# Kernel optimization log

Measured on AMD Instinct MI355X. Metric: run time of the kernel, lower is better.

## Reference

```python
import jax, jax.numpy as jnp
import numpy as np

D_MODEL = 1024
N_HEAD = 16
HEAD_SIZE = D_MODEL // N_HEAD
LAYER_ID = 12
N_LAYER = 24
HEAD_SIZE_DIVISOR = 8
TM_DIM = 32   # TIME_MIX_EXTRA_DIM
TD_DIM = 64   # TIME_DECAY_EXTRA_DIM
B, T = 4, 1024
EPS = 1e-5 * HEAD_SIZE_DIVISOR ** 2


def setup_inputs() -> dict:
    key = jax.random.key(0)
    ks = jax.random.split(key, 12)
    C = D_MODEL
    r0 = LAYER_ID / (N_LAYER - 1)
    r1 = 1.0 - LAYER_ID / N_LAYER
    ddd = np.arange(C, dtype=np.float64) / C
    time_maa_x = (1.0 - ddd ** r1).astype(np.float32)
    time_maa_w = (1.0 - ddd ** r1).astype(np.float32)
    time_maa_k = (1.0 - ddd ** r1).astype(np.float32)
    time_maa_v = (1.0 - (ddd ** r1 + 0.3 * r0)).astype(np.float32)
    time_maa_r = (1.0 - ddd ** (0.5 * r1)).astype(np.float32)
    time_maa_g = (1.0 - ddd ** (0.5 * r1)).astype(np.float32)
    n = np.arange(C, dtype=np.float64)
    time_decay = (-6.0 + 5.0 * (n / (C - 1)) ** (0.7 + 1.3 * r0)).astype(np.float32)
    zig = ((n + 1) % 3 - 1) * 0.1
    time_faaaa = (r0 * (1 - n / (C - 1)) + zig).astype(np.float32).reshape(N_HEAD, HEAD_SIZE)
    s = 1.0 / np.sqrt(C)
    inp = {
        "x": jax.random.normal(ks[0], (B, T, C), jnp.float32),
        "time_maa_x": jnp.asarray(time_maa_x),
        "time_maa_w": jnp.asarray(time_maa_w),
        "time_maa_k": jnp.asarray(time_maa_k),
        "time_maa_v": jnp.asarray(time_maa_v),
        "time_maa_r": jnp.asarray(time_maa_r),
        "time_maa_g": jnp.asarray(time_maa_g),
        "time_maa_w1": jax.random.uniform(ks[1], (C, TM_DIM * 5), jnp.float32, -0.01, 0.01),
        "time_maa_w2": jax.random.uniform(ks[2], (5, TM_DIM, C), jnp.float32, -0.01, 0.01),
        "time_decay": jnp.asarray(time_decay),
        "time_decay_w1": jax.random.uniform(ks[3], (C, TD_DIM), jnp.float32, -0.01, 0.01),
        "time_decay_w2": jax.random.uniform(ks[4], (TD_DIM, C), jnp.float32, -0.01, 0.01),
        "time_faaaa": jnp.asarray(time_faaaa),
        "W_r": jax.random.normal(ks[5], (C, C), jnp.float32) * s,
        "W_k": jax.random.normal(ks[6], (C, C), jnp.float32) * s,
        "W_v": jax.random.normal(ks[7], (C, C), jnp.float32) * s,
        "W_g": jax.random.normal(ks[8], (C, C), jnp.float32) * s,
        "W_o": jax.random.normal(ks[9], (C, C), jnp.float32) * s,
        "ln_gamma": jnp.ones((C,), jnp.float32),
        "ln_beta": jnp.zeros((C,), jnp.float32),
    }
    return inp


def _wkv6(r, k, v, w, u):
    # r,k,v,w: (B,T,H,K); u: (H,K). Sequential data-dependent linear attention.
    Bc, Tc, H, K = r.shape
    wdec = jnp.exp(-jnp.exp(w))  # decay in (0,1)

    def step(S, inp):
        r_t, k_t, v_t, wd_t = inp           # each (B,H,K)
        kv = k_t[:, :, :, None] * v_t[:, :, None, :]   # (B,H,K,K) key x value
        y = jnp.einsum('bhk,bhkj->bhj', r_t, S + u[None, :, :, None] * kv)
        S = S * wd_t[:, :, :, None] + kv    # decay along key dim, then accumulate
        return S, y

    S0 = jnp.zeros((Bc, H, K, K), r.dtype)
    xs = (jnp.swapaxes(r, 0, 1), jnp.swapaxes(k, 0, 1),
          jnp.swapaxes(v, 0, 1), jnp.swapaxes(wdec, 0, 1))
    _, ys = jax.lax.scan(step, S0, xs)      # ys: (T,B,H,K)
    return jnp.swapaxes(ys, 0, 1).reshape(Bc, Tc, H * K)


def reference(x, time_maa_x, time_maa_w, time_maa_k, time_maa_v, time_maa_r,
              time_maa_g, time_maa_w1, time_maa_w2, time_decay, time_decay_w1,
              time_decay_w2, time_faaaa, W_r, W_k, W_v, W_g, W_o, ln_gamma, ln_beta):
    Bc, Tc, C = x.shape
    H, K = N_HEAD, HEAD_SIZE
    # token shift: state[t] = x[t-1], zero at t=0
    xs = jnp.pad(x, ((0, 0), (1, 0), (0, 0)))[:, :-1]
    xx = xs - x
    # LoRA-style data-dependent mixing coefficients
    xxx = x + xx * time_maa_x
    m = jnp.tanh(xxx @ time_maa_w1).reshape(Bc, Tc, 5, TM_DIM)
    m = jnp.einsum('btfe,fec->fbtc', m, time_maa_w2)  # (5,B,T,C)
    mw, mk, mv, mr, mg = m[0], m[1], m[2], m[3], m[4]
    xw = x + xx * (time_maa_w + mw)
    xk = x + xx * (time_maa_k + mk)
    xv = x + xx * (time_maa_v + mv)
    xr = x + xx * (time_maa_r + mr)
    xg = x + xx * (time_maa_g + mg)
    r = xr @ W_r
    k = xk @ W_k
    v = xv @ W_v
    g = jax.nn.silu(xg @ W_g)
    w = time_decay + jnp.tanh(xw @ time_decay_w1) @ time_decay_w2
    y = _wkv6(r.reshape(Bc, Tc, H, K), k.reshape(Bc, Tc, H, K),
              v.reshape(Bc, Tc, H, K), w.reshape(Bc, Tc, H, K), time_faaaa)
    # GroupNorm with H groups over channel dim (per (b,t) position)
    yg = y.reshape(Bc, Tc, H, K)
    mu = jnp.mean(yg, axis=-1, keepdims=True)
    var = jnp.mean((yg - mu) ** 2, axis=-1, keepdims=True)
    yn = ((yg - mu) / jnp.sqrt(var + EPS)).reshape(Bc, Tc, C)
    yn = yn * ln_gamma + ln_beta
    return (yn * g) @ W_o
```

## Files before the change

### kernel.cpp

```cpp
#include <hip/hip_runtime.h>

#define Bb 4
#define Tt 1024
#define Cc 1024
#define Hh 16
#define BT (Bb*Tt)
#define CHUNK 32
#define NCH (Tt/CHUNK)

typedef unsigned int uint;
typedef unsigned short u16;
typedef __bf16 bf16x8 __attribute__((ext_vector_type(8)));
typedef float f32x4 __attribute__((ext_vector_type(4)));
typedef const __attribute__((address_space(1))) uint GU;
typedef __attribute__((address_space(3))) uint LU;

__device__ __forceinline__ float blo(uint u) { return __uint_as_float(u << 16); }
__device__ __forceinline__ float bhi(uint u) { return __uint_as_float(u & 0xffff0000u); }
__device__ __forceinline__ float b2f(u16 u) { return __uint_as_float(((uint)u) << 16); }
__device__ __forceinline__ u16 f2b(float f) {
  uint u = __float_as_uint(f);
  return (u16)((u + 0x7fffu + ((u >> 16) & 1u)) >> 16);
}
__device__ __forceinline__ float fast_tanh(float x) {
  float e = __expf(2.f * x);
  return 1.f - 2.f / (e + 1.f);
}

__global__ __launch_bounds__(256) void prep_xxx(const float* __restrict__ x,
    const float* __restrict__ maa_x, u16* __restrict__ xxx)
{
  int idx = blockIdx.x*256 + threadIdx.x;
  int c4 = idx & 255;
  int bt = idx >> 8;
  int t = bt & (Tt-1);
  float4 xc = ((const float4*)x)[idx];
  float4 xp = make_float4(0.f,0.f,0.f,0.f);
  if (t > 0) xp = ((const float4*)x)[idx - 256];
  float4 mx = ((const float4*)maa_x)[c4];
  ushort4 o;
  o.x = f2b(fmaf(xp.x - xc.x, mx.x, xc.x));
  o.y = f2b(fmaf(xp.y - xc.y, mx.y, xc.y));
  o.z = f2b(fmaf(xp.z - xc.z, mx.z, xc.z));
  o.w = f2b(fmaf(xp.w - xc.w, mx.w, xc.w));
  ((ushort4*)xxx)[idx] = o;
}

__global__ __launch_bounds__(256) void mix_mfma(
    const float* __restrict__ x, const float* __restrict__ m1p,
    const u16* __restrict__ w2T,
    const float* __restrict__ maa_w, const float* __restrict__ maa_k,
    const float* __restrict__ maa_v, const float* __restrict__ maa_r,
    const float* __restrict__ maa_g,
    u16* __restrict__ xw, u16* __restrict__ xk, u16* __restrict__ xv,
    u16* __restrict__ xr, u16* __restrict__ xg)
{
  __shared__ __align__(16) u16 strip[4][16][72];
  const int tid = threadIdx.x;
  const int lane = tid & 63;
  const int wv = tid >> 6;
  const int sid = blockIdx.x*4 + wv;
  const int rs = sid >> 4, cs = sid & 15;
  const int r0 = rs*16, c0 = cs*64;
  const int fr = lane & 15, kc = lane >> 4;

  float xc[4][4], xd[4][4];
  #pragma unroll
  for (int n = 0; n < 4; ++n) {
    int col = c0 + n*16 + fr;
    #pragma unroll
    for (int q = 0; q < 4; ++q) {
      int row = r0 + kc*4 + q;
      size_t o = (size_t)row*Cc + col;
      float v = x[o];
      float p = ((row & (Tt-1)) != 0) ? x[o - Cc] : 0.f;
      xc[n][q] = v;
      xd[n][q] = p - v;
    }
  }

  const size_t aBase = (size_t)(r0 + fr)*160 + kc*8;
  u16* const outs[5] = {xw, xk, xv, xr, xg};
  const float* const maas[5] = {maa_w, maa_k, maa_v, maa_r, maa_g};

  #pragma unroll
  for (int f = 0; f < 5; ++f) {
    float s8[8] = {0.f,0.f,0.f,0.f,0.f,0.f,0.f,0.f};
    #pragma unroll
    for (int z = 0; z < 4; ++z) {
      const float4* p = (const float4*)(m1p + (size_t)z*655360 + aBase + f*32);
      float4 a = p[0], b = p[1];
      s8[0]+=a.x; s8[1]+=a.y; s8[2]+=a.z; s8[3]+=a.w;
      s8[4]+=b.x; s8[5]+=b.y; s8[6]+=b.z; s8[7]+=b.w;
    }
    u16 t8[8];
    #pragma unroll
    for (int j = 0; j < 8; ++j) t8[j] = f2b(fast_tanh(s8[j]));
    bf16x8 af = *(const bf16x8*)t8;
    f32x4 acc[4];
    #pragma unroll
    for (int n = 0; n < 4; ++n) {
      bf16x8 bg = *(const bf16x8*)(w2T + (size_t)(c0 + n*16 + fr)*160 + f*32 + kc*8);
      acc[n] = __builtin_amdgcn_mfma_f32_16x16x32_bf16(af, bg, f32x4{0.f,0.f,0.f,0.f}, 0, 0, 0);
    }
    const float* __restrict__ ma = maas[f];
    u16* __restrict__ op = outs[f];
    #pragma unroll
    for (int n = 0; n < 4; ++n) {
      int colL = n*16 + fr;
      float mv = ma[c0 + colL];
      #pragma unroll
      for (int q = 0; q < 4; ++q)
        strip[wv][kc*4 + q][colL] = f2b(fmaf(xd[n][q], mv + acc[n][q], xc[n][q]));
    }
    #pragma unroll
    for (int rd = 0; rd < 2; ++rd) {
      int r8 = (lane >> 3) + rd*8;
      uint4 v = *(const uint4*)&strip[wv][r8][(lane & 7)*8];
      *(uint4*)(op + (size_t)(r0 + r8)*Cc + c0 + (lane & 7)*8) = v;
    }
  }
}

struct WPair { const float* s; u16* d; int K; int N; };
struct WPack { WPair p[9]; };

__global__ __launch_bounds__(256) void transW(WPack wp) {
  WPair pr = wp.p[blockIdx.z];
  int c0 = blockIdx.x*32, r0 = blockIdx.y*32;
  if (c0 >= pr.N || r0 >= pr.K) return;
  __shared__ float tile[32][33];
  int tc = threadIdx.x & 31, tr = threadIdx.x >> 5;
  #pragma unroll
  for (int p = 0; p < 4; ++p)
    tile[tr + p*8][tc] = pr.s[(size_t)(r0 + tr + p*8)*pr.N + c0 + tc];
  __syncthreads();
  #pragma unroll
  for (int p = 0; p < 4; ++p) {
    int n = tr + p*8;
    pr.d[(size_t)(c0 + n)*pr.K + r0 + tc] = f2b(tile[tc][n]);
  }
}

template<bool OUTF32>
__device__ __forceinline__ void mfma_core(
    const u16* __restrict__ A, const u16* __restrict__ Bt,
    void* __restrict__ Cout, const float* __restrict__ bias,
    int ld, int kloop, int N, int act)
{
  __shared__ __align__(16) u16 lds[2][2][128*32];
  const int tid = threadIdx.x;
  const int lane = tid & 63;
  const int wv = __builtin_amdgcn_readfirstlane(tid >> 6);

  const int nby8 = gridDim.y >> 3;
  const int i_lin = blockIdx.y * gridDim.x + blockIdx.x;
  const int cx = i_lin & 7, rest = i_lin >> 3;
  const int bm = (cx * nby8 + rest % nby8) * 128;
  const int bn = (rest / nby8) * 128;

  const int wm = (wv >> 1) * 64;
  const int wn = (wv & 1) * 64;
  const int kc = lane >> 4;
  const int fr = lane & 15;

  const int srow = wv*16 + (lane >> 2);
  const int ssw  = (srow >> 1) & 3;
  const int scol = ((lane & 3) ^ ssw) * 8;
  const size_t aoff = (size_t)(bm + srow) * ld + scol;
  const size_t boff = (size_t)(bn + srow) * ld + scol;

#define STAGE(bufi, kt) do { \
    size_t ko_ = (size_t)(kt) * 32; \
    __builtin_amdgcn_global_load_lds((GU*)(A + aoff + ko_), \
        (LU*)&lds[bufi][0][wv*512], 16, 0, 0); \
    __builtin_amdgcn_global_load_lds((GU*)(A + aoff + (size_t)64*ld + ko_), \
        (LU*)&lds[bufi][0][wv*512 + 64*32], 16, 0, 0); \
    __builtin_amdgcn_global_load_lds((GU*)(Bt + boff + ko_), \
        (LU*)&lds[bufi][1][wv*512], 16, 0, 0); \
    __builtin_amdgcn_global_load_lds((GU*)(Bt + boff + (size_t)64*ld + ko_), \
        (LU*)&lds[bufi][1][wv*512 + 64*32], 16, 0, 0); \
  } while(0)

  int ard[4], brd[4];
  #pragma unroll
  for (int m = 0; m < 4; ++m) {
    int ra = wm + m*16 + fr;
    int rb = wn + m*16 + fr;
    ard[m] = ra*32 + (kc ^ ((ra >> 1) & 3))*8;
    brd[m] = rb*32 + (kc ^ ((rb >> 1) & 3))*8;
  }

  f32x4 acc[4][4];
  #pragma unroll
  for (int m = 0; m < 4; ++m)
    #pragma unroll
    for (int n = 0; n < 4; ++n)
      acc[m][n] = f32x4{0.f, 0.f, 0.f, 0.f};

  const int NK = kloop >> 5;
  STAGE(0, 0);
  __syncthreads();
  int buf = 0;
  for (int kt = 0; kt < NK; ++kt) {
    if (kt + 1 < NK) STAGE(buf^1, kt+1);
    bf16x8 af[4], bg[4];
    #pragma unroll
    for (int m = 0; m < 4; ++m) af[m] = *(const bf16x8*)&lds[buf][0][ard[m]];
    #pragma unroll
    for (int n = 0; n < 4; ++n) bg[n] = *(const bf16x8*)&lds[buf][1][brd[n]];
    #pragma unroll
    for (int m = 0; m < 4; ++m)
      #pragma unroll
      for (int n = 0; n < 4; ++n)
        acc[m][n] = __builtin_amdgcn_mfma_f32_16x16x32_bf16(af[m], bg[n], acc[m][n], 0, 0, 0);
    __syncthreads();
    buf ^= 1;
  }
#undef STAGE

  const int orow = bm + wm + (lane >> 4) * 4;
  const int ocol = bn + wn + fr;
  #pragma unroll
  for (int m = 0; m < 4; ++m) {
    #pragma unroll
    for (int n = 0; n < 4; ++n) {
      int col = ocol + n*16;
      if (col < N) {
        float bs = bias ? bias[col] : 0.f;
        #pragma unroll
        for (int q = 0; q < 4; ++q) {
          float vv = acc[m][n][q] + bs;
          if (act == 1) vv = tanhf(vv);
          else if (act == 2) vv = vv / (1.f + __expf(-vv));
          else if (act == 3) vv = __expf(-__expf(vv));
          else if (act == 4) vv = __expf(vv);
          size_t off = (size_t)(orow + m*16 + q) * N + col;
          if (OUTF32) ((float*)Cout)[off] = vv;
          else ((u16*)Cout)[off] = f2b(vv);
        }
      }
    }
  }
}

template<int ACT, bool OUTF32>
__global__ __launch_bounds__(256) void gemm_mfma(
    const u16* __restrict__ A, const u16* __restrict__ Bt,
    void* __restrict__ Cout, const float* __restrict__ bias, int K, int N)
{
  mfma_core<OUTF32>(A, Bt, Cout, bias, K, K, N, ACT);
}

__global__ __launch_bounds__(256) void gemm_ksplit(
    const u16* __restrict__ A, const u16* __restrict__ Bt,
    float* __restrict__ Cp, int ld, int ksz, int N)
{
  const int z = blockIdx.z;
  mfma_core<true>(A + (size_t)z*ksz, Bt + (size_t)z*ksz,
                  Cp + (size_t)z*4096*N, nullptr, ld, ksz, N, 0);
}

__global__ __launch_bounds__(256) void gemm_ew64(
    const float* __restrict__ wl1p, const u16* __restrict__ Bt,
    const float* __restrict__ tdecay, float* __restrict__ ew)
{
  const int tid = threadIdx.x;
  const int lane = tid & 63;
  const int wv = tid >> 6;
  const int nby8 = gridDim.y >> 3;
  const int i_lin = blockIdx.y * gridDim.x + blockIdx.x;
  const int cx = i_lin & 7, rest = i_lin >> 3;
  const int bm = (cx * nby8 + rest % nby8) * 128;
  const int bn = (rest / nby8) * 128;
  const int wm = (wv >> 1) * 64;
  const int wn = (wv & 1) * 64;
  const int kc = lane >> 4;
  const int fr = lane & 15;

  bf16x8 af[4][2];
  #pragma unroll
  for (int m = 0; m < 4; ++m) {
    int row = bm + wm + m*16 + fr;
    #pragma unroll
    for (int ks = 0; ks < 2; ++ks) {
      size_t base = (size_t)row*64 + ks*32 + kc*8;
      float s8[8] = {0.f,0.f,0.f,0.f,0.f,0.f,0.f,0.f};
      #pragma unroll
      for (int z = 0; z < 4; ++z) {
        const float4* p = (const float4*)(wl1p + (size_t)z*262144 + base);
        float4 a = p[0], b = p[1];
        s8[0]+=a.x; s8[1]+=a.y; s8[2]+=a.z; s8[3]+=a.w;
        s8[4]+=b.x; s8[5]+=b.y; s8[6]+=b.z; s8[7]+=b.w;
      }
      u16 t8[8];
      #pragma unroll
      for (int j = 0; j < 8; ++j) t8[j] = f2b(fast_tanh(s8[j]));
      af[m][ks] = *(const bf16x8*)t8;
    }
  }

  f32x4 acc[4][4];
  #pragma unroll
  for (int m = 0; m < 4; ++m)
    #pragma unroll
    for (int n = 0; n < 4; ++n)
      acc[m][n] = f32x4{0.f,0.f,0.f,0.f};

  #pragma unroll
  for (int ks = 0; ks < 2; ++ks) {
    bf16x8 bg[4];
    #pragma unroll
    for (int n = 0; n < 4; ++n)
      bg[n] = *(const bf16x8*)(Bt + (size_t)(bn + wn + n*16 + fr)*64 + ks*32 + kc*8);
    #pragma unroll
    for (int m = 0; m < 4; ++m)
      #pragma unroll
      for (int n = 0; n < 4; ++n)
        acc[m][n] = __builtin_amdgcn_mfma_f32_16x16x32_bf16(af[m][ks], bg[n], acc[m][n], 0, 0, 0);
  }

  const int orow = bm + wm + kc*4;
  const int ocol = bn + wn + fr;
  #pragma unroll
  for (int n = 0; n < 4; ++n) {
    int col = ocol + n*16;
    float bs = tdecay[col];
    #pragma unroll
    for (int m = 0; m < 4; ++m)
      #pragma unroll
      for (int q = 0; q < 4; ++q)
        ew[(size_t)(orow + m*16 + q)*Cc + col] = __expf(acc[m][n][q] + bs);
  }
}

struct GPack { const u16* A[4]; const u16* B[4]; u16* C[4]; };

#define VMW(n) asm volatile("s_waitcnt vmcnt(" #n ")" ::: "memory")
#define LGKM0() asm volatile("s_waitcnt lgkmcnt(0)" ::: "memory")
#define SCHB() __builtin_amdgcn_sched_barrier(0)
#define HBAR() __builtin_amdgcn_s_barrier()

__global__ __launch_bounds__(512) void gemm_rkvg256(GPack gp) {
  __shared__ __align__(16) u16 lds[2][2][2][8192];
  const int z = blockIdx.z;
  const u16* __restrict__ Ap  = gp.A[z];
  const u16* __restrict__ Btp = gp.B[z];
  u16* __restrict__ Cp = gp.C[z];
  const int act = (z == 3) ? 2 : 0;

  const int tid = threadIdx.x;
  const int lane = tid & 63;
  const int wv = __builtin_amdgcn_readfirstlane(tid >> 6);

  const int i_lin = blockIdx.y * gridDim.x + blockIdx.x;
  const int tile = (i_lin & 7) * 8 + (i_lin >> 3);
  const int bm = (tile >> 2) * 256;
  const int bn = (tile & 3) * 256;

  const int wm = (wv >> 2) * 128;
  const int wn = (wv & 3) * 64;
  const int kc = lane >> 4;
  const int fr = lane & 15;

  const int srow0 = (wv*2 + 0)*16 + (lane >> 2);
  const int srow1 = (wv*2 + 1)*16 + (lane >> 2);
  const int sc0 = ((lane & 3) ^ ((srow0 >> 1) & 3)) * 8;
  const int sc1 = ((lane & 3) ^ ((srow1 >> 1) & 3)) * 8;
  const size_t aoff0 = (size_t)(bm + srow0)*Cc + sc0;
  const size_t aoff1 = (size_t)(bm + srow1)*Cc + sc1;
  const size_t boff0 = (size_t)(bn + srow0)*Cc + sc0;
  const size_t boff1 = (size_t)(bn + srow1)*Cc + sc1;

  int ard[8], brd[4];
  #pragma unroll
  for (int mh = 0; mh < 2; ++mh)
    #pragma unroll
    for (int mf = 0; mf < 4; ++mf) {
      int r = wm + mh*64 + mf*16 + fr;
      ard[mh*4+mf] = r*32 + (kc ^ ((r >> 1) & 3))*8;
    }
  #pragma unroll
  for (int nf = 0; nf < 4; ++nf) {
    int r = wn + nf*16 + fr;
    brd[nf] = r*32 + (kc ^ ((r >> 1) & 3))*8;
  }

  f32x4 acc[8][4];
  #pragma unroll
  for (int m = 0; m < 8; ++m)
    #pragma unroll
    for (int n = 0; n < 4; ++n)
      acc[m][n] = f32x4{0.f, 0.f, 0.f, 0.f};

#define STG256(DB, MAT, KH, kt, off0, off1, src) do { \
    u16* dst_ = &lds[(DB)][(MAT)][(KH)][wv*1024]; \
    __builtin_amdgcn_global_load_lds((GU*)((src) + (off0) + (size_t)(kt)*64 + (KH)*32), \
        (LU*)dst_, 16, 0, 0); \
    __builtin_amdgcn_global_load_lds((GU*)((src) + (off1) + (size_t)(kt)*64 + (KH)*32), \
        (LU*)(dst_ + 512), 16, 0, 0); \
  } while(0)

#define PH256(cur, KH, MH, LOADB, STMAT, STKH, DOSTAGE, VMTOK) do { \
    _Pragma("unroll") \
    for (int mf = 0; mf < 4; ++mf) \
      af[mf] = *(const bf16x8*)&lds[(cur)][0][KH][ard[(MH)*4+mf]]; \
    if (LOADB) { \
      _Pragma("unroll") \
      for (int nf = 0; nf < 4; ++nf) \
        bg[nf] = *(const bf16x8*)&lds[(cur)][1][KH][brd[nf]]; \
    } \
    if (DOSTAGE) { \
      if ((STMAT) == 0) STG256((cur)^1, 0, STKH, t+1, aoff0, aoff1, Ap); \
      else              STG256((cur)^1, 1, STKH, t+1, boff0, boff1, Btp); \
    } \
    VMTOK; \
    SCHB(); \
    HBAR(); \
    LGKM0(); \
    SCHB(); \
    __builtin_amdgcn_s_setprio(1); \
    _Pragma("unroll") \
    for (int mf = 0; mf < 4; ++mf) \
      _Pragma("unroll") \
      for (int nf = 0; nf < 4; ++nf) \
        acc[(MH)*4+mf][nf] = __builtin_amdgcn_mfma_f32_16x16x32_bf16(af[mf], bg[nf], acc[(MH)*4+mf][nf], 0, 0, 0); \
    __builtin_amdgcn_s_setprio(0); \
    SCHB(); \
    HBAR(); \
  } while(0)

  const int NK = Cc >> 6;

  STG256(0, 0, 0, 0, aoff0, aoff1, Ap);
  STG256(0, 1, 0, 0, boff0, boff1, Btp);
  STG256(0, 0, 1, 0, aoff0, aoff1, Ap);
  STG256(0, 1, 1, 0, boff0, boff1, Btp);
  VMW(4);
  SCHB();
  HBAR();

  bf16x8 af[4], bg[4];
  int t;
  #pragma unroll 2
  for (t = 0; t < NK - 1; ++t) {
    const int cur = t & 1;
    PH256(cur, 0, 0, true,  0, 0, true,  (void)0);
    PH256(cur, 0, 1, false, 1, 0, true,  VMW(4));
    PH256(cur, 1, 0, true,  0, 1, true,  (void)0);
    PH256(cur, 1, 1, false, 1, 1, true,  VMW(4));
  }
  {
    const int cur = t & 1;
    PH256(cur, 0, 0, true,  0, 0, false, (void)0);
    PH256(cur, 0, 1, false, 0, 0, false, VMW(0));
    PH256(cur, 1, 0, true,  0, 0, false, (void)0);
    PH256(cur, 1, 1, false, 0, 0, false, (void)0);
  }
#undef PH256
#undef STG256

  const int orow = bm + wm + (lane >> 4) * 4;
  const int ocol = bn + wn + fr;
  #pragma unroll
  for (int m = 0; m < 8; ++m) {
    #pragma unroll
    for (int nf = 0; nf < 4; ++nf) {
      #pragma unroll
      for (int q = 0; q < 4; ++q) {
        float vv = acc[m][nf][q];
        if (act == 2) vv = vv / (1.f + __expf(-vv));
        Cp[(size_t)(orow + (m >> 2)*64 + (m & 3)*16 + q) * Cc + ocol + nf*16] = f2b(vv);
      }
    }
  }
}

__global__ __launch_bounds__(256) void wkv_pass1(u16* __restrict__ r,
    const u16* __restrict__ k, const u16* __restrict__ v,
    const float* __restrict__ ew, const float* __restrict__ u,
    u16* __restrict__ y, u16* __restrict__ S, float* __restrict__ D)
{
  __shared__ __align__(16) u16 rS[CHUNK][72];
  __shared__ __align__(16) u16 kS[CHUNK][72];
  __shared__ __align__(16) u16 vS[CHUNK][72];
  __shared__ __align__(16) float bufEW[CHUNK][68];
  __shared__ __align__(16) float eKnL[CHUNK][68];
  __shared__ __align__(16) u16 Rt[CHUNK][72];
  __shared__ __align__(16) u16 Kt[CHUNK][72];
  __shared__ __align__(16) u16 Ru[CHUNK][72];
  __shared__ __align__(16) u16 KhT[64][40];
  __shared__ __align__(16) u16 VT[64][40];
  __shared__ __align__(16) u16 A_lds[CHUNK][40];
  __shared__ float uL[64];
  __shared__ float Dl[64];

  const int blk = blockIdx.x;
  const int chunk = blk & (NCH-1);
  const int bh = blk >> 5;
  const int h = bh & (Hh-1);
  const int b = bh >> 4;
  const int tid = threadIdx.x;
  const int lane = tid & 63;
  const int wv = tid >> 6;
  const int fr = lane & 15;
  const int kc = lane >> 4;

  const size_t rowbase = ((size_t)(b*Tt + chunk*CHUNK))*Cc + h*64;
  {
    int tt = tid >> 3, c8 = (tid & 7)*8;
    size_t go = rowbase + (size_t)tt*Cc + c8;
    *(uint4*)&rS[tt][c8] = *(const uint4*)(r + go);
    *(uint4*)&kS[tt][c8] = *(const uint4*)(k + go);
    *(uint4*)&vS[tt][c8] = *(const uint4*)(v + go);
    *(float4*)&bufEW[tt][c8]   = *(const float4*)(ew + go);
    *(float4*)&bufEW[tt][c8+4] = *(const float4*)(ew + go + 4);
  }
  if (tid < 64) uL[tid] = u[h*64 + tid];
  __syncthreads();

  if (tid < 64) {
    float eR = 1.f;
    for (int t = 0; t < CHUNK; ++t) {
      float e = bufEW[t][tid];
      bufEW[t][tid] = eR;
      eR *= __expf(-e);
      eKnL[t][tid] = __builtin_amdgcn_rcpf(eR);
    }
    Dl[tid] = eR;
    D[(size_t)blk*64 + tid] = eR;
  }
  __syncthreads();

  {
    int t = tid >> 3, i0 = (tid & 7)*8;
    uint4 rv4 = *(const uint4*)&rS[t][i0];
    uint4 kv4 = *(const uint4*)&kS[t][i0];
    const uint* rw = (const uint*)&rv4;
    const uint* kw = (const uint*)&kv4;
    u16 rt8[8], kt8[8], ru8[8];
    #pragma unroll
    for (int q = 0; q < 8; ++q) {
      int i = i0 + q;
      float rv = (q & 1) ? bhi(rw[q>>1]) : blo(rw[q>>1]);
      float kv = (q & 1) ? bhi(kw[q>>1]) : blo(kw[q>>1]);
      float eR = bufEW[t][i];
      float eKn = eKnL[t][i];
      float ktv = kv * eKn;
      rt8[q] = f2b(rv * eR);
      kt8[q] = f2b(ktv);
      ru8[q] = f2b(rv * uL[i]);
      KhT[i][t] = f2b(ktv * Dl[i]);
      VT[i][t] = vS[t][i];
    }
    *(uint4*)&Rt[t][i0] = *(const uint4*)rt8;
    *(uint4*)&Kt[t][i0] = *(const uint4*)kt8;
    *(uint4*)&Ru[t][i0] = *(const uint4*)ru8;
  }
  __syncthreads();

  {
    const int wr = wv >> 1, wc = wv & 1;
    f32x4 accA = {0.f,0.f,0.f,0.f};
    f32x4 accD = {0.f,0.f,0.f,0.f};
    #pragma unroll
    for (int ks = 0; ks < 2; ++ks) {
      bf16x8 a  = *(const bf16x8*)&Rt[wr*16+fr][kc*8 + ks*32];
      bf16x8 bb = *(const bf16x8*)&Kt[wc*16+fr][kc*8 + ks*32];
      accA = __builtin_amdgcn_mfma_f32_16x16x32_bf16(a, bb, accA, 0, 0, 0);
      bf16x8 a2 = *(const bf16x8*)&Ru[wr*16+fr][kc*8 + ks*32];
      bf16x8 b2 = *(const bf16x8*)&kS[wc*16+fr][kc*8 + ks*32];
      accD = __builtin_amdgcn_mfma_f32_16x16x32_bf16(a2, b2, accD, 0, 0, 0);
    }
    #pragma unroll
    for (int q = 0; q < 4; ++q) {
      int trow = wr*16 + kc*4 + q;
      int scol = wc*16 + fr;
      float val = (scol < trow) ? accA[q] : ((scol == trow) ? accD[q] : 0.f);
      A_lds[trow][scol] = f2b(val);
    }
  }
  __syncthreads();

  #pragma unroll
  for (int tb = 0; tb < 2; ++tb) {
    bf16x8 a  = *(const bf16x8*)&A_lds[tb*16+fr][kc*8];
    bf16x8 bb = *(const bf16x8*)&VT[wv*16+fr][kc*8];
    f32x4 acc = {0.f,0.f,0.f,0.f};
    acc = __builtin_amdgcn_mfma_f32_16x16x32_bf16(a, bb, acc, 0, 0, 0);
    #pragma unroll
    for (int q = 0; q < 4; ++q) {
      int t = tb*16 + kc*4 + q;
      int j = wv*16 + fr;
      y[rowbase + (size_t)t*Cc + j] = f2b(acc[q]);
    }
  }
  #pragma unroll
  for (int jb = 0; jb < 4; ++jb) {
    bf16x8 a  = *(const bf16x8*)&KhT[wv*16+fr][kc*8];
    bf16x8 bb = *(const bf16x8*)&VT[jb*16+fr][kc*8];
    f32x4 acc = {0.f,0.f,0.f,0.f};
    acc = __builtin_amdgcn_mfma_f32_16x16x32_bf16(a, bb, acc, 0, 0, 0);
    #pragma unroll
    for (int q = 0; q < 4; ++q) {
      int i = wv*16 + kc*4 + q;
      int j = jb*16 + fr;
      S[((size_t)blk*64 + i)*64 + j] = f2b(acc[q]);
    }
  }
  {
    int tt = tid >> 3, c8 = (tid & 7)*8;
    *(uint4*)(r + rowbase + (size_t)tt*Cc + c8) = *(const uint4*)&Rt[tt][c8];
  }
}

__global__ __launch_bounds__(256) void wkv_pass2(u16* __restrict__ S,
    const float* __restrict__ D)
{
  __shared__ float Dl[NCH][64];
  const int bh = blockIdx.x;
  const int tid = threadIdx.x;
  {
    const float4* src = (const float4*)(D + (size_t)bh*NCH*64);
    float4* dst = (float4*)&Dl[0][0];
    dst[tid] = src[tid];
    dst[tid + 256] = src[tid + 256];
  }
  __syncthreads();
  const int j = tid & 63, i0 = (tid >> 6)*16;
  float Sr[16];
  #pragma unroll
  for (int ii = 0; ii < 16; ++ii) Sr[ii] = 0.f;
  for (int c = 0; c < NCH; ++c) {
    size_t base = (((size_t)bh*NCH + c)*64 + i0)*64 + j;
    u16 tmp[16];
    #pragma unroll
    for (int ii = 0; ii < 16; ++ii) tmp[ii] = S[base + ii*64];
    #pragma unroll
    for (int ii = 0; ii < 16; ++ii) S[base + ii*64] = f2b(Sr[ii]);
    #pragma unroll
    for (int ii = 0; ii < 16; ++ii) Sr[ii] = fmaf(Sr[ii], Dl[c][i0+ii], b2f(tmp[ii]));
  }
}

__global__ __launch_bounds__(256) void gn_gate(const u16* __restrict__ y,
   const u16* __restrict__ g, const u16* __restrict__ rc, const u16* __restrict__ S,
   const float* __restrict__ gamma, const float* __restrict__ beta, u16* __restrict__ out)
{
  __shared__ u16 rcl[8][Cc];
  const int bt0 = blockIdx.x * 8;
  const int b = bt0 >> 10;
  const int t0 = bt0 & (Tt-1);
  const int chunk = t0 >> 5;
  const int tid = threadIdx.x;
  #pragma unroll
  for (int rr = 0; rr < 8; ++rr)
    ((ushort4*)rcl[rr])[tid] = ((const ushort4*)(rc + (size_t)(bt0+rr)*Cc))[tid];
  __syncthreads();
  const int c0 = tid*4, h = c0 >> 6, j0 = c0 & 63;
  const u16* Sb = S + (((size_t)(b*Hh + h)*NCH + chunk)*64)*64 + j0;
  float corr[8][4];
  #pragma unroll
  for (int rr = 0; rr < 8; ++rr)
    #pragma unroll
    for (int q = 0; q < 4; ++q) corr[rr][q] = 0.f;
  #pragma unroll 4
  for (int i = 0; i < 64; ++i) {
    ushort4 sv = *(const ushort4*)(Sb + (size_t)i*64);
    float s0 = b2f(sv.x), s1 = b2f(sv.y), s2 = b2f(sv.z), s3 = b2f(sv.w);
    #pragma unroll
    for (int rr = 0; rr < 8; ++rr) {
      float rv = b2f(rcl[rr][h*64 + i]);
      corr[rr][0] = fmaf(rv, s0, corr[rr][0]);
      corr[rr][1] = fmaf(rv, s1, corr[rr][1]);
      corr[rr][2] = fmaf(rv, s2, corr[rr][2]);
      corr[rr][3] = fmaf(rv, s3, corr[rr][3]);
    }
  }
  float4 ga = ((const float4*)gamma)[tid];
  float4 be = ((const float4*)beta)[tid];
  #pragma unroll
  for (int rr = 0; rr < 8; ++rr) {
    size_t o4 = (size_t)(bt0+rr)*(Cc/4) + tid;
    ushort4 yv4 = ((const ushort4*)y)[o4];
    float y0 = b2f(yv4.x) + corr[rr][0];
    float y1 = b2f(yv4.y) + corr[rr][1];
    float y2 = b2f(yv4.z) + corr[rr][2];
    float y3 = b2f(yv4.w) + corr[rr][3];
    float s  = y0 + y1 + y2 + y3;
    float sq = y0*y0 + y1*y1 + y2*y2 + y3*y3;
    #pragma unroll
    for (int m = 1; m < 16; m <<= 1) {
      s  += __shfl_xor(s, m, 64);
      sq += __shfl_xor(sq, m, 64);
    }
    float mu  = s * (1.f/64.f);
    float var = sq * (1.f/64.f) - mu*mu;
    float rstd = rsqrtf(var + 6.4e-4f);
    ushort4 gu = ((const ushort4*)g)[o4];
    ushort4 ou;
    ou.x = f2b(((y0 - mu)*rstd*ga.x + be.x) * b2f(gu.x));
    ou.y = f2b(((y1 - mu)*rstd*ga.y + be.y) * b2f(gu.y));
    ou.z = f2b(((y2 - mu)*rstd*ga.z + be.z) * b2f(gu.z));
    ou.w = f2b(((y3 - mu)*rstd*ga.w + be.w) * b2f(gu.w));
    ((ushort4*)out)[o4] = ou;
  }
}

extern "C" void kernel_launch(void* const* d_in, const int* in_sizes, int n_in,
                              void* d_out, int out_size, void* d_ws, size_t ws_size,
                              hipStream_t stream) {
  const float* x      = (const float*)d_in[0];
  const float* maa_x  = (const float*)d_in[1];
  const float* maa_w  = (const float*)d_in[2];
  const float* maa_k  = (const float*)d_in[3];
  const float* maa_v  = (const float*)d_in[4];
  const float* maa_r  = (const float*)d_in[5];
  const float* maa_g  = (const float*)d_in[6];
  const float* w1     = (const float*)d_in[7];
  const float* w2     = (const float*)d_in[8];
  const float* tdecay = (const float*)d_in[9];
  const float* tdw1   = (const float*)d_in[10];
  const float* tdw2   = (const float*)d_in[11];
  const float* faaaa  = (const float*)d_in[12];
  const float* Wr     = (const float*)d_in[13];
  const float* Wk     = (const float*)d_in[14];
  const float* Wv     = (const float*)d_in[15];
  const float* Wg     = (const float*)d_in[16];
  const float* Wo     = (const float*)d_in[17];
  const float* gamma  = (const float*)d_in[18];
  const float* beta   = (const float*)d_in[19];
  float* out = (float*)d_out;

  const size_t MB = 1u << 20;
  char* wsb = (char*)d_ws;
  float* ewb  = (float*)(wsb + 0);
  float* m1p  = (float*)(wsb + 0);
  u16*   w2T  = (u16*)(wsb + 12*MB);
  u16*   xk   = (u16*)(wsb + 16*MB);
  u16*   xv   = (u16*)(wsb + 24*MB);
  u16*   xr   = (u16*)(wsb + 32*MB);
  u16*   xg   = (u16*)(wsb + 40*MB);
  u16*   xw   = (u16*)(wsb + 48*MB);
  u16*   rbuf = (u16*)(wsb + 56*MB);
  float* wl1p = (float*)(wsb + 56*MB);
  u16*   kbuf = (u16*)(wsb + 64*MB);
  u16*   vbuf = (u16*)(wsb + 72*MB);
  u16*   gbuf = (u16*)(wsb + 80*MB);
  float* Dbuf = (float*)(wsb + 88*MB);
  u16*   Sbuf = (u16*)(wsb + 16*MB);
  u16*   BW0  = (u16*)(wsb + 88*MB + 512*1024);
  u16*   BW1  = (u16*)((char*)BW0 + 2*MB);
  u16*   BW2  = (u16*)((char*)BW1 + 2*MB);
  u16*   BW3  = (u16*)((char*)BW2 + 2*MB);
  u16*   BW4  = (u16*)((char*)BW3 + 2*MB);
  u16*   w1T  = (u16*)((char*)BW4 + 2*MB);
  u16*   tdw1T = (u16*)(wsb + 99*MB);
  u16*   tdw2T = (u16*)(wsb + 99*MB + 256*1024);
  u16*   gated = xr;
  u16*   xxx16 = (u16*)d_out;
  u16*   yb16  = (u16*)d_out;

  dim3 blk(256);
  WPack wp;
  wp.p[0] = {Wr, BW0, Cc, Cc};  wp.p[1] = {Wk, BW1, Cc, Cc};
  wp.p[2] = {Wv, BW2, Cc, Cc};  wp.p[3] = {Wg, BW3, Cc, Cc};
  wp.p[4] = {Wo, BW4, Cc, Cc};  wp.p[5] = {w1, w1T, Cc, 160};
  wp.p[6] = {tdw1, tdw1T, Cc, 64}; wp.p[7] = {tdw2, tdw2T, 64, Cc};
  wp.p[8] = {w2, w2T, 160, Cc};
  transW<<<dim3(32,32,9), blk, 0, stream>>>(wp);
  prep_xxx<<<BT*Cc/4/256, blk, 0, stream>>>(x, maa_x, xxx16);
  gemm_ksplit<<<dim3(2, 32, 4), blk, 0, stream>>>(xxx16, w1T, m1p, Cc, 256, 160);
  mix_mfma<<<1024, blk, 0, stream>>>(x, m1p, w2T, maa_w, maa_k, maa_v, maa_r, maa_g,
                                     xw, xk, xv, xr, xg);
  gemm_ksplit<<<dim3(1, 32, 4), blk, 0, stream>>>(xw, tdw1T, wl1p, Cc, 256, 64);
  gemm_ew64<<<dim3(8, 32), blk, 0, stream>>>(wl1p, tdw2T, tdecay, ewb);
  GPack gp;
  gp.A[0] = xr; gp.A[1] = xk; gp.A[2] = xv; gp.A[3] = xg;
  gp.B[0] = BW0; gp.B[1] = BW1; gp.B[2] = BW2; gp.B[3] = BW3;
  gp.C[0] = rbuf; gp.C[1] = kbuf; gp.C[2] = vbuf; gp.C[3] = gbuf;
  gemm_rkvg256<<<dim3(4, 16, 4), dim3(512), 0, stream>>>(gp);
  wkv_pass1<<<Bb*Hh*NCH, blk, 0, stream>>>(rbuf, kbuf, vbuf, ewb, faaaa, yb16, Sbuf, Dbuf);
  wkv_pass2<<<Bb*Hh, blk, 0, stream>>>(Sbuf, Dbuf);
  gn_gate<<<BT/8, blk, 0, stream>>>(yb16, gbuf, rbuf, Sbuf, gamma, beta, gated);
  gemm_mfma<0,true><<<dim3(8, 32), blk, 0, stream>>>(gated, BW4, out, nullptr, Cc, Cc);
}
```

Baseline: 200.3 us.

## Fuse decay LoRA into WKV pass, merge prep kernels, widen state-scan grid

Removes the gemm_ew64 kernel and computes the per-chunk decay exp(tdecay + tanh(xw@W1)@W2) inside wkv_pass1 with a small MFMA, so the fp32 16MB ew buffer is never written to or read back from global memory. The weight transpose and xxx prep kernels are merged into one launch. wkv_pass2 is split over four times as many blocks, and its loads are hoisted so all chunk states are fetched before the sequential scan. In exchange, each WKV block redoes the k-split reduction and LoRA matmul for its own head slice, and the hoisted loads add register pressure.

New measurement: 188.9 us. 1.06x faster.

```diff
diff --git a/kernel.cpp b/kernel.cpp
--- a/kernel.cpp
+++ b/kernel.cpp
@@ -27,23 +27,45 @@
   return 1.f - 2.f / (e + 1.f);
 }
 
-__global__ __launch_bounds__(256) void prep_xxx(const float* __restrict__ x,
-    const float* __restrict__ maa_x, u16* __restrict__ xxx)
+struct WPair { const float* s; u16* d; int K; int N; };
+struct WPack { WPair p[9]; };
+
+__global__ __launch_bounds__(256) void prep_transW(WPack wp,
+    const float* __restrict__ x, const float* __restrict__ maa_x,
+    u16* __restrict__ xxx)
 {
-  int idx = blockIdx.x*256 + threadIdx.x;
-  int c4 = idx & 255;
-  int bt = idx >> 8;
-  int t = bt & (Tt-1);
-  float4 xc = ((const float4*)x)[idx];
-  float4 xp = make_float4(0.f,0.f,0.f,0.f);
-  if (t > 0) xp = ((const float4*)x)[idx - 256];
-  float4 mx = ((const float4*)maa_x)[c4];
-  ushort4 o;
-  o.x = f2b(fmaf(xp.x - xc.x, mx.x, xc.x));
-  o.y = f2b(fmaf(xp.y - xc.y, mx.y, xc.y));
-  o.z = f2b(fmaf(xp.z - xc.z, mx.z, xc.z));
-  o.w = f2b(fmaf(xp.w - xc.w, mx.w, xc.w));
-  ((ushort4*)xxx)[idx] = o;
+  __shared__ float tile[32][33];
+  if (blockIdx.z < 9) {
+    WPair pr = wp.p[blockIdx.z];
+    int c0 = blockIdx.x*32, r0 = blockIdx.y*32;
+    if (c0 >= pr.N || r0 >= pr.K) return;
+    int tc = threadIdx.x & 31, tr = threadIdx.x >> 5;
+    #pragma unroll
+    for (int p = 0; p < 4; ++p)
+      tile[tr + p*8][tc] = pr.s[(size_t)(r0 + tr + p*8)*pr.N + c0 + tc];
+    __syncthreads();
+    #pragma unroll
+    for (int p = 0; p < 4; ++p) {
+      int n = tr + p*8;
+      pr.d[(size_t)(c0 + n)*pr.K + r0 + tc] = f2b(tile[tc][n]);
+    }
+  } else {
+    int vb = (blockIdx.z - 9)*1024 + blockIdx.y*32 + blockIdx.x;
+    int idx = vb*256 + threadIdx.x;
+    int c4 = idx & 255;
+    int bt = idx >> 8;
+    int t = bt & (Tt-1);
+    float4 xc = ((const float4*)x)[idx];
+    float4 xp = make_float4(0.f,0.f,0.f,0.f);
+    if (t > 0) xp = ((const float4*)x)[idx - 256];
+    float4 mx = ((const float4*)maa_x)[c4];
+    ushort4 o;
+    o.x = f2b(fmaf(xp.x - xc.x, mx.x, xc.x));
+    o.y = f2b(fmaf(xp.y - xc.y, mx.y, xc.y));
+    o.z = f2b(fmaf(xp.z - xc.z, mx.z, xc.z));
+    o.w = f2b(fmaf(xp.w - xc.w, mx.w, xc.w));
+    ((ushort4*)xxx)[idx] = o;
+  }
 }
 
 __global__ __launch_bounds__(256) void mix_mfma(
@@ -122,26 +144,6 @@
   }
 }
 
-struct WPair { const float* s; u16* d; int K; int N; };
-struct WPack { WPair p[9]; };
-
-__global__ __launch_bounds__(256) void transW(WPack wp) {
-  WPair pr = wp.p[blockIdx.z];
-  int c0 = blockIdx.x*32, r0 = blockIdx.y*32;
-  if (c0 >= pr.N || r0 >= pr.K) return;
-  __shared__ float tile[32][33];
-  int tc = threadIdx.x & 31, tr = threadIdx.x >> 5;
-  #pragma unroll
-  for (int p = 0; p < 4; ++p)
-    tile[tr + p*8][tc] = pr.s[(size_t)(r0 + tr + p*8)*pr.N + c0 + tc];
-  __syncthreads();
-  #pragma unroll
-  for (int p = 0; p < 4; ++p) {
-    int n = tr + p*8;
-    pr.d[(size_t)(c0 + n)*pr.K + r0 + tc] = f2b(tile[tc][n]);
-  }
-}
-
 template<bool OUTF32>
 __device__ __forceinline__ void mfma_core(
     const u16* __restrict__ A, const u16* __restrict__ Bt,
@@ -233,8 +235,6 @@
           float vv = acc[m][n][q] + bs;
           if (act == 1) vv = tanhf(vv);
           else if (act == 2) vv = vv / (1.f + __expf(-vv));
-          else if (act == 3) vv = __expf(-__expf(vv));
-          else if (act == 4) vv = __expf(vv);
           size_t off = (size_t)(orow + m*16 + q) * N + col;
           if (OUTF32) ((float*)Cout)[off] = vv;
           else ((u16*)Cout)[off] = f2b(vv);
@@ -259,79 +259,6 @@
   const int z = blockIdx.z;
   mfma_core<true>(A + (size_t)z*ksz, Bt + (size_t)z*ksz,
                   Cp + (size_t)z*4096*N, nullptr, ld, ksz, N, 0);
-}
-
-__global__ __launch_bounds__(256) void gemm_ew64(
-    const float* __restrict__ wl1p, const u16* __restrict__ Bt,
-    const float* __restrict__ tdecay, float* __restrict__ ew)
-{
-  const int tid = threadIdx.x;
-  const int lane = tid & 63;
-  const int wv = tid >> 6;
-  const int nby8 = gridDim.y >> 3;
-  const int i_lin = blockIdx.y * gridDim.x + blockIdx.x;
-  const int cx = i_lin & 7, rest = i_lin >> 3;
-  const int bm = (cx * nby8 + rest % nby8) * 128;
-  const int bn = (rest / nby8) * 128;
-  const int wm = (wv >> 1) * 64;
-  const int wn = (wv & 1) * 64;
-  const int kc = lane >> 4;
-  const int fr = lane & 15;
-
-  bf16x8 af[4][2];
-  #pragma unroll
-  for (int m = 0; m < 4; ++m) {
-    int row = bm + wm + m*16 + fr;
-    #pragma unroll
-    for (int ks = 0; ks < 2; ++ks) {
-      size_t base = (size_t)row*64 + ks*32 + kc*8;
-      float s8[8] = {0.f,0.f,0.f,0.f,0.f,0.f,0.f,0.f};
-      #pragma unroll
-      for (int z = 0; z < 4; ++z) {
-        const float4* p = (const float4*)(wl1p + (size_t)z*262144 + base);
-        float4 a = p[0], b = p[1];
-        s8[0]+=a.x; s8[1]+=a.y; s8[2]+=a.z; s8[3]+=a.w;
-        s8[4]+=b.x; s8[5]+=b.y; s8[6]+=b.z; s8[7]+=b.w;
-      }
-      u16 t8[8];
-      #pragma unroll
-      for (int j = 0; j < 8; ++j) t8[j] = f2b(fast_tanh(s8[j]));
-      af[m][ks] = *(const bf16x8*)t8;
-    }
-  }
-
-  f32x4 acc[4][4];
-  #pragma unroll
-  for (int m = 0; m < 4; ++m)
-    #pragma unroll
-    for (int n = 0; n < 4; ++n)
-      acc[m][n] = f32x4{0.f,0.f,0.f,0.f};
-
-  #pragma unroll
-  for (int ks = 0; ks < 2; ++ks) {
-    bf16x8 bg[4];
-    #pragma unroll
-    for (int n = 0; n < 4; ++n)
-      bg[n] = *(const bf16x8*)(Bt + (size_t)(bn + wn + n*16 + fr)*64 + ks*32 + kc*8);
-    #pragma unroll
-    for (int m = 0; m < 4; ++m)
-      #pragma unroll
-      for (int n = 0; n < 4; ++n)
-        acc[m][n] = __builtin_amdgcn_mfma_f32_16x16x32_bf16(af[m][ks], bg[n], acc[m][n], 0, 0, 0);
-  }
-
-  const int orow = bm + wm + kc*4;
-  const int ocol = bn + wn + fr;
-  #pragma unroll
-  for (int n = 0; n < 4; ++n) {
-    int col = ocol + n*16;
-    float bs = tdecay[col];
-    #pragma unroll
-    for (int m = 0; m < 4; ++m)
-      #pragma unroll
-      for (int q = 0; q < 4; ++q)
-        ew[(size_t)(orow + m*16 + q)*Cc + col] = __expf(acc[m][n][q] + bs);
-  }
 }
 
 struct GPack { const u16* A[4]; const u16* B[4]; u16* C[4]; };
@@ -478,12 +405,14 @@
 
 __global__ __launch_bounds__(256) void wkv_pass1(u16* __restrict__ r,
     const u16* __restrict__ k, const u16* __restrict__ v,
-    const float* __restrict__ ew, const float* __restrict__ u,
+    const float* __restrict__ wl1p, const u16* __restrict__ tdw2T,
+    const float* __restrict__ tdecay, const float* __restrict__ u,
     u16* __restrict__ y, u16* __restrict__ S, float* __restrict__ D)
 {
   __shared__ __align__(16) u16 rS[CHUNK][72];
   __shared__ __align__(16) u16 kS[CHUNK][72];
   __shared__ __align__(16) u16 vS[CHUNK][72];
+  __shared__ __align__(16) u16 aW[CHUNK][72];
   __shared__ __align__(16) float bufEW[CHUNK][68];
   __shared__ __align__(16) float eKnL[CHUNK][68];
   __shared__ __align__(16) u16 Rt[CHUNK][72];
@@ -506,17 +435,48 @@
   const int fr = lane & 15;
   const int kc = lane >> 4;
 
-  const size_t rowbase = ((size_t)(b*Tt + chunk*CHUNK))*Cc + h*64;
+  const int trow0 = b*Tt + chunk*CHUNK;
+  const size_t rowbase = (size_t)trow0*Cc + h*64;
   {
     int tt = tid >> 3, c8 = (tid & 7)*8;
     size_t go = rowbase + (size_t)tt*Cc + c8;
     *(uint4*)&rS[tt][c8] = *(const uint4*)(r + go);
     *(uint4*)&kS[tt][c8] = *(const uint4*)(k + go);
     *(uint4*)&vS[tt][c8] = *(const uint4*)(v + go);
-    *(float4*)&bufEW[tt][c8]   = *(const float4*)(ew + go);
-    *(float4*)&bufEW[tt][c8+4] = *(const float4*)(ew + go + 4);
+    size_t wrow = (size_t)(trow0 + tt)*64 + c8;
+    float s8[8] = {0.f,0.f,0.f,0.f,0.f,0.f,0.f,0.f};
+    #pragma unroll
+    for (int z = 0; z < 4; ++z) {
+      const float4* p = (const float4*)(wl1p + (size_t)z*262144 + wrow);
+      float4 a = p[0], b2 = p[1];
+      s8[0]+=a.x; s8[1]+=a.y; s8[2]+=a.z; s8[3]+=a.w;
+      s8[4]+=b2.x; s8[5]+=b2.y; s8[6]+=b2.z; s8[7]+=b2.w;
+    }
+    u16 t8[8];
+    #pragma unroll
+    for (int j = 0; j < 8; ++j) t8[j] = f2b(fast_tanh(s8[j]));
+    *(uint4*)&aW[tt][c8] = *(const uint4*)t8;
   }
   if (tid < 64) uL[tid] = u[h*64 + tid];
+  __syncthreads();
+
+  {
+    const int icol = wv*16 + fr;
+    const float bs = tdecay[h*64 + icol];
+    #pragma unroll
+    for (int tb = 0; tb < 2; ++tb) {
+      f32x4 acc = {0.f,0.f,0.f,0.f};
+      #pragma unroll
+      for (int ks = 0; ks < 2; ++ks) {
+        bf16x8 a  = *(const bf16x8*)&aW[tb*16+fr][kc*8 + ks*32];
+        bf16x8 bb = *(const bf16x8*)(tdw2T + (size_t)(h*64 + icol)*64 + ks*32 + kc*8);
+        acc = __builtin_amdgcn_mfma_f32_16x16x32_bf16(a, bb, acc, 0, 0, 0);
+      }
+      #pragma unroll
+      for (int q = 0; q < 4; ++q)
+        bufEW[tb*16 + kc*4 + q][icol] = __expf(acc[q] + bs);
+    }
+  }
   __syncthreads();
 
   if (tid < 64) {
@@ -618,7 +578,8 @@
     const float* __restrict__ D)
 {
   __shared__ float Dl[NCH][64];
-  const int bh = blockIdx.x;
+  const int bh = blockIdx.x >> 2;
+  const int jq = blockIdx.x & 3;
   const int tid = threadIdx.x;
   {
     const float4* src = (const float4*)(D + (size_t)bh*NCH*64);
@@ -627,19 +588,25 @@
     dst[tid + 256] = src[tid + 256];
   }
   __syncthreads();
-  const int j = tid & 63, i0 = (tid >> 6)*16;
-  float Sr[16];
-  #pragma unroll
-  for (int ii = 0; ii < 16; ++ii) Sr[ii] = 0.f;
+  const int j = jq*16 + (tid & 15);
+  const int i0 = (tid >> 4) * 4;
+  const size_t base0 = (((size_t)bh*NCH)*64 + i0)*64 + j;
+  u16 tmp[NCH][4];
+  #pragma unroll
   for (int c = 0; c < NCH; ++c) {
-    size_t base = (((size_t)bh*NCH + c)*64 + i0)*64 + j;
-    u16 tmp[16];
-    #pragma unroll
-    for (int ii = 0; ii < 16; ++ii) tmp[ii] = S[base + ii*64];
-    #pragma unroll
-    for (int ii = 0; ii < 16; ++ii) S[base + ii*64] = f2b(Sr[ii]);
-    #pragma unroll
-    for (int ii = 0; ii < 16; ++ii) Sr[ii] = fmaf(Sr[ii], Dl[c][i0+ii], b2f(tmp[ii]));
+    size_t base = base0 + (size_t)c*4096;
+    #pragma unroll
+    for (int ii = 0; ii < 4; ++ii) tmp[c][ii] = S[base + ii*64];
+  }
+  float Sr[4] = {0.f, 0.f, 0.f, 0.f};
+  #pragma unroll
+  for (int c = 0; c < NCH; ++c) {
+    size_t base = base0 + (size_t)c*4096;
+    #pragma unroll
+    for (int ii = 0; ii < 4; ++ii) {
+      S[base + ii*64] = f2b(Sr[ii]);
+      Sr[ii] = fmaf(Sr[ii], Dl[c][i0+ii], b2f(tmp[c][ii]));
+    }
   }
 }
 
@@ -734,8 +701,8 @@
 
   const size_t MB = 1u << 20;
   char* wsb = (char*)d_ws;
-  float* ewb  = (float*)(wsb + 0);
   float* m1p  = (float*)(wsb + 0);
+  float* wl1p = (float*)(wsb + 0);
   u16*   w2T  = (u16*)(wsb + 12*MB);
   u16*   xk   = (u16*)(wsb + 16*MB);
   u16*   xv   = (u16*)(wsb + 24*MB);
@@ -743,7 +710,6 @@
   u16*   xg   = (u16*)(wsb + 40*MB);
   u16*   xw   = (u16*)(wsb + 48*MB);
   u16*   rbuf = (u16*)(wsb + 56*MB);
-  float* wl1p = (float*)(wsb + 56*MB);
   u16*   kbuf = (u16*)(wsb + 64*MB);
   u16*   vbuf = (u16*)(wsb + 72*MB);
   u16*   gbuf = (u16*)(wsb + 80*MB);
@@ -768,20 +734,19 @@
   wp.p[4] = {Wo, BW4, Cc, Cc};  wp.p[5] = {w1, w1T, Cc, 160};
   wp.p[6] = {tdw1, tdw1T, Cc, 64}; wp.p[7] = {tdw2, tdw2T, 64, Cc};
   wp.p[8] = {w2, w2T, 160, Cc};
-  transW<<<dim3(32,32,9), blk, 0, stream>>>(wp);
-  prep_xxx<<<BT*Cc/4/256, blk, 0, stream>>>(x, maa_x, xxx16);
+  prep_transW<<<dim3(32,32,13), blk, 0, stream>>>(wp, x, maa_x, xxx16);
   gemm_ksplit<<<dim3(2, 32, 4), blk, 0, stream>>>(xxx16, w1T, m1p, Cc, 256, 160);
   mix_mfma<<<1024, blk, 0, stream>>>(x, m1p, w2T, maa_w, maa_k, maa_v, maa_r, maa_g,
                                      xw, xk, xv, xr, xg);
   gemm_ksplit<<<dim3(1, 32, 4), blk, 0, stream>>>(xw, tdw1T, wl1p, Cc, 256, 64);
-  gemm_ew64<<<dim3(8, 32), blk, 0, stream>>>(wl1p, tdw2T, tdecay, ewb);
   GPack gp;
   gp.A[0] = xr; gp.A[1] = xk; gp.A[2] = xv; gp.A[3] = xg;
   gp.B[0] = BW0; gp.B[1] = BW1; gp.B[2] = BW2; gp.B[3] = BW3;
   gp.C[0] = rbuf; gp.C[1] = kbuf; gp.C[2] = vbuf; gp.C[3] = gbuf;
   gemm_rkvg256<<<dim3(4, 16, 4), dim3(512), 0, stream>>>(gp);
-  wkv_pass1<<<Bb*Hh*NCH, blk, 0, stream>>>(rbuf, kbuf, vbuf, ewb, faaaa, yb16, Sbuf, Dbuf);
-  wkv_pass2<<<Bb*Hh, blk, 0, stream>>>(Sbuf, Dbuf);
+  wkv_pass1<<<Bb*Hh*NCH, blk, 0, stream>>>(rbuf, kbuf, vbuf, wl1p, tdw2T, tdecay,
+                                           faaaa, yb16, Sbuf, Dbuf);
+  wkv_pass2<<<Bb*Hh*4, blk, 0, stream>>>(Sbuf, Dbuf);
   gn_gate<<<BT/8, blk, 0, stream>>>(yb16, gbuf, rbuf, Sbuf, gamma, beta, gated);
   gemm_mfma<0,true><<<dim3(8, 32), blk, 0, stream>>>(gated, BW4, out, nullptr, Cc, Cc);
 }
```
